# Performance work log

Hardware: AMD Instinct MI355X
Metric: run time of the kernel (lower is better)

## Reference

```python
import jax, jax.numpy as jnp
import numpy as np

DIM = 512  # DIM_IMAGE_EMBEDDING
HEAD = 64
B, T = 16, 2048


def setup_inputs() -> dict:
    key = jax.random.key(0)
    ks = jax.random.split(key, 8)
    s = 1.0 / np.sqrt(DIM)
    return {
        'x': jax.random.normal(ks[0], (B, T, DIM), jnp.float32),
        'Wq': jax.random.normal(ks[1], (HEAD, DIM), jnp.float32) * s,
        'Wk': jax.random.normal(ks[2], (HEAD, DIM), jnp.float32) * s,
        'Wv': jax.random.normal(ks[3], (HEAD, DIM), jnp.float32) * s,
        'fx_real': jax.random.normal(ks[4], (T, HEAD // 4), jnp.float32),
        'fx_imag': jax.random.normal(ks[5], (T, HEAD // 4), jnp.float32),
        'fy_real': jax.random.normal(ks[6], (T, HEAD // 4), jnp.float32),
        'fy_imag': jax.random.normal(ks[7], (T, HEAD // 4), jnp.float32),
    }


def _rotate_half(t, fr, fi):
    # t: [B, T, H/2] viewed as H/4 complex pairs; fr, fi: [T, H/4]
    b, s, d = t.shape
    tc = t.reshape(b, s, d // 2, 2)
    a, bb = tc[..., 0], tc[..., 1]
    ro = a * fr - bb * fi  # real part of complex product
    io = a * fi + bb * fr  # imag part
    return jnp.stack([ro, io], axis=-1).reshape(b, s, d)


def apply_rotary_2d(t, fx_real, fx_imag, fy_real, fy_imag):
    h = t.shape[-1] // 2
    vx = _rotate_half(t[..., :h], fx_real, fx_imag)
    vy = _rotate_half(t[..., h:], fy_real, fy_imag)
    return jnp.concatenate([vx, vy], axis=-1)


def reference(x, Wq, Wk, Wv, fx_real, fx_imag, fy_real, fy_imag):
    C = x.shape[-1]
    q = jnp.einsum('btc,hc->bth', x, Wq)
    k = jnp.einsum('btc,hc->bth', x, Wk)
    v = jnp.einsum('btc,hc->bth', x, Wv)
    q = apply_rotary_2d(q, fx_real, fx_imag, fy_real, fy_imag)
    k = apply_rotary_2d(k, fx_real, fx_imag, fy_real, fy_imag)
    # NOTE: original scales by input dim C (=512), not head_size
    wei = jnp.einsum('bqh,bkh->bqk', q, k) / jnp.sqrt(jnp.float32(C))
    softwei = jax.nn.softmax(wei, axis=-1)
    out = jnp.einsum('bqk,bkh->bqh', softwei, v)
    return out
```

## Files before the change

kernel.cpp:

```cpp
#include <hip/hip_runtime.h>
#include <hip/hip_bf16.h>

#define BB 16
#define TT 2048
#define DIMC 512
#define HEADH 64

typedef __attribute__((ext_vector_type(8))) short short8v;
typedef __attribute__((ext_vector_type(4))) float f32x4;

static __device__ __forceinline__ unsigned short f2bf(float f) {
    __hip_bfloat16 h = __float2bfloat16(f);
    unsigned short u;
    __builtin_memcpy(&u, &h, 2);
    return u;
}
static __device__ __forceinline__ unsigned int packbf(float lo, float hi) {
    float2 f2; f2.x = lo; f2.y = hi;
    __hip_bfloat162 h2 = __float22bfloat162_rn(f2);
    unsigned int u;
    __builtin_memcpy(&u, &h2, 4);
    return u;
}
#define EXP2R __builtin_amdgcn_exp2f
static __device__ __forceinline__ void async_copy16(void* lds, const void* g) {
    __builtin_amdgcn_global_load_lds(
        (const __attribute__((address_space(1))) unsigned char*)g,
        (__attribute__((address_space(3))) unsigned char*)lds, 16, 0, 0);
}

union bfrag {
    unsigned int u[4];
    short8v v;
};

__global__ __launch_bounds__(256) void wcvt_kernel(
    const float* __restrict__ Wq, const float* __restrict__ Wk,
    const float* __restrict__ Wv, unsigned short* __restrict__ wb)
{
    const int idx = blockIdx.x * 256 + threadIdx.x;
    const int e   = idx << 3;
    const int row = e >> 9, col = e & 511;
    const float* src = (row < 64) ? Wq : (row < 128) ? Wk : Wv;
    const float* p = src + (size_t)(row & 63) * DIMC + col;
    float4 a = *(const float4*)p;
    float4 b = *(const float4*)(p + 4);
    uint4 o;
    o.x = packbf(a.x, a.y); o.y = packbf(a.z, a.w);
    o.z = packbf(b.x, b.y); o.w = packbf(b.z, b.w);
    *(uint4*)(wb + e) = o;
}

__global__ __launch_bounds__(256, 2) void qkv_mfma_kernel(
    const float* __restrict__ x,
    const unsigned short* __restrict__ wb,
    const float* __restrict__ fxr, const float* __restrict__ fxi,
    const float* __restrict__ fyr, const float* __restrict__ fyi,
    unsigned short* __restrict__ qo, unsigned short* __restrict__ ko,
    unsigned short* __restrict__ vt)
{
    __shared__ unsigned char xlds[16384];

    const int tid = threadIdx.x;
    const int w   = tid >> 6;
    const int l   = tid & 63;
    const int q   = l & 15;
    const int g   = l >> 4;
    const int t0  = blockIdx.x << 6;

    f32x4 acc[3][4];
    #pragma unroll
    for (int j = 0; j < 3; ++j)
        #pragma unroll
        for (int tt = 0; tt < 4; ++tt) acc[j][tt] = (f32x4){0.f, 0.f, 0.f, 0.f};

    const unsigned short* wp0 = wb + ((size_t)((3 * w + 0) * 16 + q)) * DIMC + 8 * g;
    const unsigned short* wp1 = wb + ((size_t)((3 * w + 1) * 16 + q)) * DIMC + 8 * g;
    const unsigned short* wp2 = wb + ((size_t)((3 * w + 2) * 16 + q)) * DIMC + 8 * g;

    const int rl = l >> 3;
    const int cb = (l & 7) ^ rl;
    const float* xsrc0 = x + (size_t)(t0 + 16 * w + 0 + rl) * DIMC + 4 * cb;
    const float* xsrc1 = x + (size_t)(t0 + 16 * w + 8 + rl) * DIMC + 4 * cb;
    unsigned char* xdst0 = xlds + (16 * w + 0) * 128;
    unsigned char* xdst1 = xlds + (16 * w + 8) * 128;

#define STAGE_X(bufsel, k0) do {                                              \
        async_copy16(xdst0 + (bufsel) * 8192, xsrc0 + (k0));                  \
        async_copy16(xdst1 + (bufsel) * 8192, xsrc1 + (k0));                  \
    } while (0)

    STAGE_X(0, 0);
    __syncthreads();

    int cur = 0;
    for (int it = 0; it < 16; ++it) {
        const int k0 = it << 5;
        if (it < 15) STAGE_X(cur ^ 1, k0 + 32);

        short8v wf0 = *(const short8v*)(wp0 + k0);
        short8v wf1 = *(const short8v*)(wp1 + k0);
        short8v wf2 = *(const short8v*)(wp2 + k0);

        const unsigned char* xb = xlds + cur * 8192;
        #pragma unroll
        for (int tt = 0; tt < 4; ++tt) {
            const int rr = tt * 16 + q;
            const int s0 = (2 * g)     ^ (q & 7);
            const int s1 = (2 * g + 1) ^ (q & 7);
            float4 f0 = *(const float4*)(xb + rr * 128 + s0 * 16);
            float4 f1 = *(const float4*)(xb + rr * 128 + s1 * 16);
            bfrag xv;
            xv.u[0] = packbf(f0.x, f0.y); xv.u[1] = packbf(f0.z, f0.w);
            xv.u[2] = packbf(f1.x, f1.y); xv.u[3] = packbf(f1.z, f1.w);
            acc[0][tt] = __builtin_amdgcn_mfma_f32_16x16x32_bf16(wf0, xv.v, acc[0][tt], 0, 0, 0);
            acc[1][tt] = __builtin_amdgcn_mfma_f32_16x16x32_bf16(wf1, xv.v, acc[1][tt], 0, 0, 0);
            acc[2][tt] = __builtin_amdgcn_mfma_f32_16x16x32_bf16(wf2, xv.v, acc[2][tt], 0, 0, 0);
        }

        __syncthreads();
        cur ^= 1;
    }

    const float qscale = 1.4426950408889634f / 22.627416997969522f;
    #pragma unroll
    for (int j = 0; j < 3; ++j) {
        const int gt   = 3 * w + j;
        const int mat  = gt >> 2;
        const int hbase = (gt & 3) * 16 + 4 * g;
        #pragma unroll
        for (int tt = 0; tt < 4; ++tt) {
            const int trow = t0 + tt * 16 + q;
            const int tl   = trow & (TT - 1);
            if (mat == 2) {
                const int b = trow >> 11;
                #pragma unroll
                for (int r = 0; r < 4; ++r)
                    vt[((size_t)(b * HEADH) + hbase + r) * TT + tl] = f2bf(acc[j][tt][r]);
            } else {
                const float sc = (mat == 0) ? qscale : 1.f;
                unsigned short* dst = ((mat == 0) ? qo : ko) + (size_t)trow * HEADH;
                const int half = hbase >> 5;
                const float* frt = half ? fyr : fxr;
                const float* fit = half ? fyi : fxi;
                const int pi0 = (hbase & 31) >> 1;
                float fr0 = frt[tl * 16 + pi0],     fi0 = fit[tl * 16 + pi0];
                float fr1 = frt[tl * 16 + pi0 + 1], fi1 = fit[tl * 16 + pi0 + 1];
                float e0 = acc[j][tt][0] * fr0 - acc[j][tt][1] * fi0;
                float e1 = acc[j][tt][0] * fi0 + acc[j][tt][1] * fr0;
                float e2 = acc[j][tt][2] * fr1 - acc[j][tt][3] * fi1;
                float e3 = acc[j][tt][2] * fi1 + acc[j][tt][3] * fr1;
                uint2 ow;
                ow.x = packbf(e0 * sc, e1 * sc);
                ow.y = packbf(e2 * sc, e3 * sc);
                *(uint2*)(dst + hbase) = ow;
            }
        }
    }
#undef STAGE_X
}

__global__ __launch_bounds__(256, 2) void attn_mfma_kernel(
    const unsigned short* __restrict__ qws,
    const unsigned short* __restrict__ kws,
    const unsigned short* __restrict__ vtw,
    float* __restrict__ out)
{
    __shared__ unsigned char smem[40960];

    const int tid = threadIdx.x;
    const int w   = tid >> 6;
    const int l   = tid & 63;
    const int q   = l & 15;
    const int g   = l >> 4;
    const int b   = blockIdx.x >> 5;
    const int q0  = (blockIdx.x & 31) << 6;
    const int qw  = q0 + 16 * w;
    const int rx  = q & 7;
    const int swz = (q & 7) << 2;

    const int rl = l >> 3;
    const int sl = (l & 7) ^ rl;

    unsigned int* pldsw = (unsigned int*)(smem + 32768 + (w << 11));

    const unsigned short* kbase = kws + (size_t)b * TT * HEADH;
    const unsigned short* vbase = vtw + (size_t)b * HEADH * TT;

    const unsigned short* ksrc0 = kbase + (size_t)(16 * w + rl) * HEADH + 8 * sl;
    const unsigned short* ksrc1 = kbase + (size_t)(16 * w + 8 + rl) * HEADH + 8 * sl;
    const unsigned short* vsrc0 = vbase + (size_t)(16 * w + rl) * TT + 8 * sl;
    const unsigned short* vsrc1 = vbase + (size_t)(16 * w + 8 + rl) * TT + 8 * sl;

#define STAGE_TILE(bufsel, kv)  do {                                          \
        unsigned char* kd = smem + (bufsel) * 8192 + (w << 11);               \
        unsigned char* vd = smem + 16384 + (bufsel) * 8192 + (w << 11);       \
        async_copy16(kd,        ksrc0 + (size_t)(kv) * HEADH);                \
        async_copy16(kd + 1024, ksrc1 + (size_t)(kv) * HEADH);                \
        async_copy16(vd,        vsrc0 + (kv));                                \
        async_copy16(vd + 1024, vsrc1 + (kv));                                \
    } while (0)

    short8v qf0, qf1;
    {
        const unsigned short* qp = qws + ((size_t)(b * TT + qw + q)) * HEADH + 8 * g;
        qf0 = *(const short8v*)(qp);
        qf1 = *(const short8v*)(qp + 32);
    }

    f32x4 oacc[4];
    #pragma unroll
    for (int mt = 0; mt < 4; ++mt) oacc[mt] = (f32x4){0.f, 0.f, 0.f, 0.f};
    float m = -1e30f, lsum = 0.f;

    STAGE_TILE(0, 0);
    __syncthreads();

    int cur = 0;
    for (int it = 0; it < 32; ++it) {
        if (it < 31) STAGE_TILE(cur ^ 1, (it + 1) << 6);

        const unsigned char* kb = smem + cur * 8192;
        const unsigned char* vb = smem + 16384 + cur * 8192;

        f32x4 sacc[4];
        #pragma unroll
        for (int n = 0; n < 4; ++n) {
            const int r = 16 * n + q;
            const short8v k0 = *(const short8v*)(kb + r * 128 + ((g ^ rx) << 4));
            const short8v k1 = *(const short8v*)(kb + r * 128 + (((4 + g) ^ rx) << 4));
            f32x4 z = (f32x4){0.f, 0.f, 0.f, 0.f};
            z = __builtin_amdgcn_mfma_f32_16x16x32_bf16(k0, qf0, z, 0, 0, 0);
            z = __builtin_amdgcn_mfma_f32_16x16x32_bf16(k1, qf1, z, 0, 0, 0);
            sacc[n] = z;
        }

        float cmax = sacc[0][0];
        #pragma unroll
        for (int n = 0; n < 4; ++n)
            #pragma unroll
            for (int r = 0; r < 4; ++r) cmax = fmaxf(cmax, sacc[n][r]);
        cmax = fmaxf(cmax, __shfl_xor(cmax, 16));
        cmax = fmaxf(cmax, __shfl_xor(cmax, 32));
        const float mnew = fmaxf(m, cmax);

        float p[4][4];
        float psum = 0.f;
        #pragma unroll
        for (int n = 0; n < 4; ++n)
            #pragma unroll
            for (int r = 0; r < 4; ++r) {
                p[n][r] = EXP2R(sacc[n][r] - mnew);
                psum += p[n][r];
            }
        psum += __shfl_xor(psum, 16);
        psum += __shfl_xor(psum, 32);

        const float sc = EXP2R(m - mnew);
        if (__any(cmax > m)) {
            #pragma unroll
            for (int mt = 0; mt < 4; ++mt)
                #pragma unroll
                for (int r = 0; r < 4; ++r) oacc[mt][r] *= sc;
        }
        lsum = lsum * sc + psum;
        m = mnew;

        #pragma unroll
        for (int n = 0; n < 4; ++n) {
            uint2 wv;
            wv.x = packbf(p[n][0], p[n][1]);
            wv.y = packbf(p[n][2], p[n][3]);
            *(uint2*)&pldsw[q * 32 + ((8 * n + 2 * g) ^ swz)] = wv;
        }

        #pragma unroll
        for (int s = 0; s < 2; ++s) {
            const short8v pb = *(const short8v*)&pldsw[q * 32 + ((16 * s + 4 * g) ^ swz)];
            #pragma unroll
            for (int mt = 0; mt < 4; ++mt) {
                const int d = 16 * mt + q;
                const short8v vfr = *(const short8v*)(vb + d * 128 + ((((s << 2) + g) ^ rx) << 4));
                oacc[mt] = __builtin_amdgcn_mfma_f32_16x16x32_bf16(vfr, pb, oacc[mt], 0, 0, 0);
            }
        }

        __syncthreads();
        cur ^= 1;
    }

    const float inv = 1.f / lsum;
    float* op = out + ((size_t)(b * TT + qw + q)) * HEADH;
    #pragma unroll
    for (int mt = 0; mt < 4; ++mt) {
        float4 v4 = make_float4(oacc[mt][0] * inv, oacc[mt][1] * inv,
                                oacc[mt][2] * inv, oacc[mt][3] * inv);
        *(float4*)(op + 16 * mt + 4 * g) = v4;
    }
#undef STAGE_TILE
}

extern "C" void kernel_launch(void* const* d_in, const int* in_sizes, int n_in,
                              void* d_out, int out_size, void* d_ws, size_t ws_size,
                              hipStream_t stream)
{
    const float* x   = (const float*)d_in[0];
    const float* Wq  = (const float*)d_in[1];
    const float* Wk  = (const float*)d_in[2];
    const float* Wv  = (const float*)d_in[3];
    const float* fxr = (const float*)d_in[4];
    const float* fxi = (const float*)d_in[5];
    const float* fyr = (const float*)d_in[6];
    const float* fyi = (const float*)d_in[7];
    float* out = (float*)d_out;

    unsigned short* qo = (unsigned short*)d_ws;
    unsigned short* ko = qo + (size_t)BB * TT * HEADH;
    unsigned short* vt = ko + (size_t)BB * TT * HEADH;
    unsigned short* wb = vt + (size_t)BB * TT * HEADH;

    wcvt_kernel<<<48, 256, 0, stream>>>(Wq, Wk, Wv, wb);
    qkv_mfma_kernel<<<(BB * TT) / 64, 256, 0, stream>>>(x, wb, fxr, fxi, fyr, fyi,
                                                        qo, ko, vt);
    attn_mfma_kernel<<<BB * 32, 256, 0, stream>>>(qo, ko, vt, out);
}
```

Measured before the change: 71.74 us.

## Load V fragments directly from global memory and raise attention occupancy

The attention kernel no longer stages V tiles through LDS. Each lane loads its V fragments straight from global memory into registers at the start of every iteration. This shrinks shared memory from 40KB to 24KB, and launch bounds go from 2 to 4 blocks per CU. The softmax row-sum reduction is also moved after the PV MFMAs so it can overlap them. The risk is global-load latency on the critical path before the PV MFMAs, and more register pressure under the tighter launch bound.

```diff
diff --git a/kernel.cpp b/kernel.cpp
--- a/kernel.cpp
+++ b/kernel.cpp
@@ -160,13 +160,13 @@
 #undef STAGE_X
 }
 
-__global__ __launch_bounds__(256, 2) void attn_mfma_kernel(
+__global__ __launch_bounds__(256, 4) void attn_mfma_kernel(
     const unsigned short* __restrict__ qws,
     const unsigned short* __restrict__ kws,
     const unsigned short* __restrict__ vtw,
     float* __restrict__ out)
 {
-    __shared__ unsigned char smem[40960];
+    __shared__ unsigned char smem[24576];
 
     const int tid = threadIdx.x;
     const int w   = tid >> 6;
@@ -182,23 +182,18 @@
     const int rl = l >> 3;
     const int sl = (l & 7) ^ rl;
 
-    unsigned int* pldsw = (unsigned int*)(smem + 32768 + (w << 11));
+    unsigned int* pldsw = (unsigned int*)(smem + 16384 + (w << 11));
 
     const unsigned short* kbase = kws + (size_t)b * TT * HEADH;
     const unsigned short* vbase = vtw + (size_t)b * HEADH * TT;
 
     const unsigned short* ksrc0 = kbase + (size_t)(16 * w + rl) * HEADH + 8 * sl;
     const unsigned short* ksrc1 = kbase + (size_t)(16 * w + 8 + rl) * HEADH + 8 * sl;
-    const unsigned short* vsrc0 = vbase + (size_t)(16 * w + rl) * TT + 8 * sl;
-    const unsigned short* vsrc1 = vbase + (size_t)(16 * w + 8 + rl) * TT + 8 * sl;
-
-#define STAGE_TILE(bufsel, kv)  do {                                          \
+
+#define STAGE_K(bufsel, kv)  do {                                             \
         unsigned char* kd = smem + (bufsel) * 8192 + (w << 11);               \
-        unsigned char* vd = smem + 16384 + (bufsel) * 8192 + (w << 11);       \
         async_copy16(kd,        ksrc0 + (size_t)(kv) * HEADH);                \
         async_copy16(kd + 1024, ksrc1 + (size_t)(kv) * HEADH);                \
-        async_copy16(vd,        vsrc0 + (kv));                                \
-        async_copy16(vd + 1024, vsrc1 + (kv));                                \
     } while (0)
 
     short8v qf0, qf1;
@@ -213,15 +208,23 @@
     for (int mt = 0; mt < 4; ++mt) oacc[mt] = (f32x4){0.f, 0.f, 0.f, 0.f};
     float m = -1e30f, lsum = 0.f;
 
-    STAGE_TILE(0, 0);
+    STAGE_K(0, 0);
     __syncthreads();
 
     int cur = 0;
     for (int it = 0; it < 32; ++it) {
-        if (it < 31) STAGE_TILE(cur ^ 1, (it + 1) << 6);
+        const int kv0 = it << 6;
+        if (it < 31) STAGE_K(cur ^ 1, kv0 + 64);
+
+        short8v vf[2][4];
+        #pragma unroll
+        for (int s = 0; s < 2; ++s)
+            #pragma unroll
+            for (int mt = 0; mt < 4; ++mt)
+                vf[s][mt] = *(const short8v*)(vbase +
+                    (size_t)(16 * mt + q) * TT + kv0 + 32 * s + 8 * g);
 
         const unsigned char* kb = smem + cur * 8192;
-        const unsigned char* vb = smem + 16384 + cur * 8192;
 
         f32x4 sacc[4];
         #pragma unroll
@@ -245,45 +248,43 @@
         const float mnew = fmaxf(m, cmax);
 
         float p[4][4];
-        float psum = 0.f;
-        #pragma unroll
-        for (int n = 0; n < 4; ++n)
-            #pragma unroll
-            for (int r = 0; r < 4; ++r) {
+        #pragma unroll
+        for (int n = 0; n < 4; ++n) {
+            #pragma unroll
+            for (int r = 0; r < 4; ++r)
                 p[n][r] = EXP2R(sacc[n][r] - mnew);
-                psum += p[n][r];
-            }
-        psum += __shfl_xor(psum, 16);
-        psum += __shfl_xor(psum, 32);
-
-        const float sc = EXP2R(m - mnew);
-        if (__any(cmax > m)) {
-            #pragma unroll
-            for (int mt = 0; mt < 4; ++mt)
-                #pragma unroll
-                for (int r = 0; r < 4; ++r) oacc[mt][r] *= sc;
-        }
-        lsum = lsum * sc + psum;
-        m = mnew;
-
-        #pragma unroll
-        for (int n = 0; n < 4; ++n) {
             uint2 wv;
             wv.x = packbf(p[n][0], p[n][1]);
             wv.y = packbf(p[n][2], p[n][3]);
             *(uint2*)&pldsw[q * 32 + ((8 * n + 2 * g) ^ swz)] = wv;
         }
 
+        const float sc = EXP2R(m - mnew);
+        if (__any(cmax > m)) {
+            #pragma unroll
+            for (int mt = 0; mt < 4; ++mt)
+                #pragma unroll
+                for (int r = 0; r < 4; ++r) oacc[mt][r] *= sc;
+        }
+
         #pragma unroll
         for (int s = 0; s < 2; ++s) {
             const short8v pb = *(const short8v*)&pldsw[q * 32 + ((16 * s + 4 * g) ^ swz)];
             #pragma unroll
-            for (int mt = 0; mt < 4; ++mt) {
-                const int d = 16 * mt + q;
-                const short8v vfr = *(const short8v*)(vb + d * 128 + ((((s << 2) + g) ^ rx) << 4));
-                oacc[mt] = __builtin_amdgcn_mfma_f32_16x16x32_bf16(vfr, pb, oacc[mt], 0, 0, 0);
-            }
-        }
+            for (int mt = 0; mt < 4; ++mt)
+                oacc[mt] = __builtin_amdgcn_mfma_f32_16x16x32_bf16(vf[s][mt], pb,
+                                                                   oacc[mt], 0, 0, 0);
+        }
+
+        float psum = 0.f;
+        #pragma unroll
+        for (int n = 0; n < 4; ++n)
+            #pragma unroll
+            for (int r = 0; r < 4; ++r) psum += p[n][r];
+        psum += __shfl_xor(psum, 16);
+        psum += __shfl_xor(psum, 32);
+        lsum = lsum * sc + psum;
+        m = mnew;
 
         __syncthreads();
         cur ^= 1;
@@ -297,7 +298,7 @@
                                 oacc[mt][2] * inv, oacc[mt][3] * inv);
         *(float4*)(op + 16 * mt + 4 * g) = v4;
     }
-#undef STAGE_TILE
+#undef STAGE_K
 }
 
 extern "C" void kernel_launch(void* const* d_in, const int* in_sizes, int n_in,
```

Result: slower. 97.07 us (+35.3%).

## Split attention KV range across two wave groups and halve QKV tile rows

Applied to the files above, without the earlier changes.

The attention kernel now runs 512 threads per block: two groups of four waves each handle half of the key/value sequence for the same 64 queries. Their partial softmax states (max, sum, output) are merged through shared memory at the end. The QKV projection kernel is retiled to 32 tokens per block, doubling the grid and raising the occupancy hint. Together these aim to expose more parallelism and latency hiding on 512 attention blocks, at the cost of doubled LDS use in attention and an extra merge phase. The softmax row-sum is also moved after the PV MFMAs so it can overlap with them.

```diff
diff --git a/kernel.cpp b/kernel.cpp
--- a/kernel.cpp
+++ b/kernel.cpp
@@ -51,7 +51,7 @@
     *(uint4*)(wb + e) = o;
 }
 
-__global__ __launch_bounds__(256, 2) void qkv_mfma_kernel(
+__global__ __launch_bounds__(256, 4) void qkv_mfma_kernel(
     const float* __restrict__ x,
     const unsigned short* __restrict__ wb,
     const float* __restrict__ fxr, const float* __restrict__ fxi,
@@ -59,20 +59,20 @@
     unsigned short* __restrict__ qo, unsigned short* __restrict__ ko,
     unsigned short* __restrict__ vt)
 {
-    __shared__ unsigned char xlds[16384];
+    __shared__ unsigned char xlds[8192];
 
     const int tid = threadIdx.x;
     const int w   = tid >> 6;
     const int l   = tid & 63;
     const int q   = l & 15;
     const int g   = l >> 4;
-    const int t0  = blockIdx.x << 6;
-
-    f32x4 acc[3][4];
+    const int t0  = blockIdx.x << 5;
+
+    f32x4 acc[3][2];
     #pragma unroll
     for (int j = 0; j < 3; ++j)
         #pragma unroll
-        for (int tt = 0; tt < 4; ++tt) acc[j][tt] = (f32x4){0.f, 0.f, 0.f, 0.f};
+        for (int tt = 0; tt < 2; ++tt) acc[j][tt] = (f32x4){0.f, 0.f, 0.f, 0.f};
 
     const unsigned short* wp0 = wb + ((size_t)((3 * w + 0) * 16 + q)) * DIMC + 8 * g;
     const unsigned short* wp1 = wb + ((size_t)((3 * w + 1) * 16 + q)) * DIMC + 8 * g;
@@ -80,15 +80,11 @@
 
     const int rl = l >> 3;
     const int cb = (l & 7) ^ rl;
-    const float* xsrc0 = x + (size_t)(t0 + 16 * w + 0 + rl) * DIMC + 4 * cb;
-    const float* xsrc1 = x + (size_t)(t0 + 16 * w + 8 + rl) * DIMC + 4 * cb;
-    unsigned char* xdst0 = xlds + (16 * w + 0) * 128;
-    unsigned char* xdst1 = xlds + (16 * w + 8) * 128;
-
-#define STAGE_X(bufsel, k0) do {                                              \
-        async_copy16(xdst0 + (bufsel) * 8192, xsrc0 + (k0));                  \
-        async_copy16(xdst1 + (bufsel) * 8192, xsrc1 + (k0));                  \
-    } while (0)
+    const float* xsrc = x + (size_t)(t0 + 8 * w + rl) * DIMC + 4 * cb;
+    unsigned char* xdst = xlds + (w << 10);
+
+#define STAGE_X(bufsel, k0) \
+        async_copy16(xdst + (bufsel) * 4096, xsrc + (k0))
 
     STAGE_X(0, 0);
     __syncthreads();
@@ -102,9 +98,9 @@
         short8v wf1 = *(const short8v*)(wp1 + k0);
         short8v wf2 = *(const short8v*)(wp2 + k0);
 
-        const unsigned char* xb = xlds + cur * 8192;
-        #pragma unroll
-        for (int tt = 0; tt < 4; ++tt) {
+        const unsigned char* xb = xlds + cur * 4096;
+        #pragma unroll
+        for (int tt = 0; tt < 2; ++tt) {
             const int rr = tt * 16 + q;
             const int s0 = (2 * g)     ^ (q & 7);
             const int s1 = (2 * g + 1) ^ (q & 7);
@@ -129,7 +125,7 @@
         const int mat  = gt >> 2;
         const int hbase = (gt & 3) * 16 + 4 * g;
         #pragma unroll
-        for (int tt = 0; tt < 4; ++tt) {
+        for (int tt = 0; tt < 2; ++tt) {
             const int trow = t0 + tt * 16 + q;
             const int tl   = trow & (TT - 1);
             if (mat == 2) {
@@ -160,43 +156,45 @@
 #undef STAGE_X
 }
 
-__global__ __launch_bounds__(256, 2) void attn_mfma_kernel(
+__global__ __launch_bounds__(512, 4) void attn_mfma_kernel(
     const unsigned short* __restrict__ qws,
     const unsigned short* __restrict__ kws,
     const unsigned short* __restrict__ vtw,
     float* __restrict__ out)
 {
-    __shared__ unsigned char smem[40960];
+    __shared__ unsigned char smem[81920];
 
     const int tid = threadIdx.x;
     const int w   = tid >> 6;
+    const int wq  = w & 3;
+    const int h   = w >> 2;
     const int l   = tid & 63;
     const int q   = l & 15;
     const int g   = l >> 4;
     const int b   = blockIdx.x >> 5;
     const int q0  = (blockIdx.x & 31) << 6;
-    const int qw  = q0 + 16 * w;
+    const int qw  = q0 + 16 * wq;
     const int rx  = q & 7;
     const int swz = (q & 7) << 2;
 
     const int rl = l >> 3;
     const int sl = (l & 7) ^ rl;
 
-    unsigned int* pldsw = (unsigned int*)(smem + 32768 + (w << 11));
+    unsigned int* pldsw = (unsigned int*)(smem + 65536 + (w << 11));
 
     const unsigned short* kbase = kws + (size_t)b * TT * HEADH;
     const unsigned short* vbase = vtw + (size_t)b * HEADH * TT;
 
-    const unsigned short* ksrc0 = kbase + (size_t)(16 * w + rl) * HEADH + 8 * sl;
-    const unsigned short* ksrc1 = kbase + (size_t)(16 * w + 8 + rl) * HEADH + 8 * sl;
-    const unsigned short* vsrc0 = vbase + (size_t)(16 * w + rl) * TT + 8 * sl;
-    const unsigned short* vsrc1 = vbase + (size_t)(16 * w + 8 + rl) * TT + 8 * sl;
+    const unsigned short* ksrc0 = kbase + (size_t)(h * 1024 + 16 * wq + rl) * HEADH + 8 * sl;
+    const unsigned short* ksrc1 = ksrc0 + (size_t)8 * HEADH;
+    const unsigned short* vsrc0 = vbase + (size_t)(16 * wq + rl) * TT + h * 1024 + 8 * sl;
+    const unsigned short* vsrc1 = vsrc0 + (size_t)8 * TT;
 
 #define STAGE_TILE(bufsel, kv)  do {                                          \
-        unsigned char* kd = smem + (bufsel) * 8192 + (w << 11);               \
-        unsigned char* vd = smem + 16384 + (bufsel) * 8192 + (w << 11);       \
+        unsigned char* kd = smem + (h << 14) + (bufsel) * 8192 + (wq << 11);  \
         async_copy16(kd,        ksrc0 + (size_t)(kv) * HEADH);                \
         async_copy16(kd + 1024, ksrc1 + (size_t)(kv) * HEADH);                \
+        unsigned char* vd = smem + 32768 + (h << 14) + (bufsel) * 8192 + (wq << 11); \
         async_copy16(vd,        vsrc0 + (kv));                                \
         async_copy16(vd + 1024, vsrc1 + (kv));                                \
     } while (0)
@@ -217,11 +215,12 @@
     __syncthreads();
 
     int cur = 0;
-    for (int it = 0; it < 32; ++it) {
-        if (it < 31) STAGE_TILE(cur ^ 1, (it + 1) << 6);
-
-        const unsigned char* kb = smem + cur * 8192;
-        const unsigned char* vb = smem + 16384 + cur * 8192;
+    for (int it = 0; it < 16; ++it) {
+        const int kv0 = it << 6;
+        if (it < 15) STAGE_TILE(cur ^ 1, kv0 + 64);
+
+        const unsigned char* kb = smem + (h << 14) + cur * 8192;
+        const unsigned char* vb = smem + 32768 + (h << 14) + cur * 8192;
 
         f32x4 sacc[4];
         #pragma unroll
@@ -245,33 +244,23 @@
         const float mnew = fmaxf(m, cmax);
 
         float p[4][4];
-        float psum = 0.f;
-        #pragma unroll
-        for (int n = 0; n < 4; ++n)
-            #pragma unroll
-            for (int r = 0; r < 4; ++r) {
+        #pragma unroll
+        for (int n = 0; n < 4; ++n) {
+            #pragma unroll
+            for (int r = 0; r < 4; ++r)
                 p[n][r] = EXP2R(sacc[n][r] - mnew);
-                psum += p[n][r];
-            }
-        psum += __shfl_xor(psum, 16);
-        psum += __shfl_xor(psum, 32);
-
-        const float sc = EXP2R(m - mnew);
-        if (__any(cmax > m)) {
-            #pragma unroll
-            for (int mt = 0; mt < 4; ++mt)
-                #pragma unroll
-                for (int r = 0; r < 4; ++r) oacc[mt][r] *= sc;
-        }
-        lsum = lsum * sc + psum;
-        m = mnew;
-
-        #pragma unroll
-        for (int n = 0; n < 4; ++n) {
             uint2 wv;
             wv.x = packbf(p[n][0], p[n][1]);
             wv.y = packbf(p[n][2], p[n][3]);
             *(uint2*)&pldsw[q * 32 + ((8 * n + 2 * g) ^ swz)] = wv;
+        }
+
+        const float sc = EXP2R(m - mnew);
+        if (__any(cmax > m)) {
+            #pragma unroll
+            for (int mt = 0; mt < 4; ++mt)
+                #pragma unroll
+                for (int r = 0; r < 4; ++r) oacc[mt][r] *= sc;
         }
 
         #pragma unroll
@@ -285,18 +274,55 @@
             }
         }
 
+        float psum = 0.f;
+        #pragma unroll
+        for (int n = 0; n < 4; ++n)
+            #pragma unroll
+            for (int r = 0; r < 4; ++r) psum += p[n][r];
+        psum += __shfl_xor(psum, 16);
+        psum += __shfl_xor(psum, 32);
+        lsum = lsum * sc + psum;
+        m = mnew;
+
         __syncthreads();
         cur ^= 1;
     }
 
-    const float inv = 1.f / lsum;
-    float* op = out + ((size_t)(b * TT + qw + q)) * HEADH;
-    #pragma unroll
-    for (int mt = 0; mt < 4; ++mt) {
-        float4 v4 = make_float4(oacc[mt][0] * inv, oacc[mt][1] * inv,
-                                oacc[mt][2] * inv, oacc[mt][3] * inv);
-        *(float4*)(op + 16 * mt + 4 * g) = v4;
-    }
+    __syncthreads();
+    float* o_f  = (float*)smem;
+    float* ml_f = (float*)(smem + 32768);
+    {
+        const int prow = h * 64 + 16 * wq + q;
+        #pragma unroll
+        for (int mt = 0; mt < 4; ++mt)
+            *(f32x4*)&o_f[prow * 64 + 16 * mt + 4 * g] = oacc[mt];
+        if (g == 0) {
+            ml_f[h * 128 + 16 * wq + q]      = m;
+            ml_f[h * 128 + 64 + 16 * wq + q] = lsum;
+        }
+    }
+    __syncthreads();
+
+    const int cq = tid >> 3;
+    const int ch = (tid & 7) << 3;
+    const float m0 = ml_f[cq],       l0 = ml_f[64 + cq];
+    const float m1 = ml_f[128 + cq], l1 = ml_f[192 + cq];
+    const float M  = fmaxf(m0, m1);
+    const float a0 = EXP2R(m0 - M), a1 = EXP2R(m1 - M);
+    const float inv = 1.f / (a0 * l0 + a1 * l1);
+    const float* o0 = &o_f[cq * 64 + ch];
+    const float* o1 = &o_f[(64 + cq) * 64 + ch];
+    float4 A0 = *(const float4*)(o0), B0 = *(const float4*)(o0 + 4);
+    float4 A1 = *(const float4*)(o1), B1 = *(const float4*)(o1 + 4);
+    float* op = out + ((size_t)(b * TT + q0 + cq)) * HEADH + ch;
+    *(float4*)(op)     = make_float4((a0 * A0.x + a1 * A1.x) * inv,
+                                     (a0 * A0.y + a1 * A1.y) * inv,
+                                     (a0 * A0.z + a1 * A1.z) * inv,
+                                     (a0 * A0.w + a1 * A1.w) * inv);
+    *(float4*)(op + 4) = make_float4((a0 * B0.x + a1 * B1.x) * inv,
+                                     (a0 * B0.y + a1 * B1.y) * inv,
+                                     (a0 * B0.z + a1 * B1.z) * inv,
+                                     (a0 * B0.w + a1 * B1.w) * inv);
 #undef STAGE_TILE
 }
 
@@ -320,7 +346,7 @@
     unsigned short* wb = vt + (size_t)BB * TT * HEADH;
 
     wcvt_kernel<<<48, 256, 0, stream>>>(Wq, Wk, Wv, wb);
-    qkv_mfma_kernel<<<(BB * TT) / 64, 256, 0, stream>>>(x, wb, fxr, fxi, fyr, fyi,
+    qkv_mfma_kernel<<<(BB * TT) / 32, 256, 0, stream>>>(x, wb, fxr, fxi, fyr, fyi,
                                                         qo, ko, vt);
-    attn_mfma_kernel<<<BB * 32, 256, 0, stream>>>(qo, ko, vt, out);
-}
+    attn_mfma_kernel<<<BB * 32, 512, 0, stream>>>(qo, ko, vt, out);
+}
```

Result: slower. 74.81 us (+4.3%).

## Split KV into four chunks per block with 32x32 MFMA and merge partial softmax

Applied to the files above, without the earlier changes.

The attention kernel now launches 512 threads per block: two query halves of 32 rows times four KV chunks of 512 keys each, an in-block split-K flash-decoding scheme. It uses 32x32x16 bf16 MFMAs instead of 16x16x32, and passes the P fragments through cross-lane shuffles instead of an LDS round trip. At the end, the per-chunk partial outputs, maxima and sums are merged through LDS. The aim is more waves per CU and fewer serial loop iterations per wave. In exchange it needs more LDS (about 66KB per block), adds an epilogue reduction, and relies on a `bfrag` type defined outside this hunk.

```diff
diff --git a/kernel.cpp b/kernel.cpp
--- a/kernel.cpp
+++ b/kernel.cpp
@@ -8,6 +8,7 @@
 
 typedef __attribute__((ext_vector_type(8))) short short8v;
 typedef __attribute__((ext_vector_type(4))) float f32x4;
+typedef __attribute__((ext_vector_type(16))) float f32x16;
 
 static __device__ __forceinline__ unsigned short f2bf(float f) {
     __hip_bfloat16 h = __float2bfloat16(f);
@@ -160,143 +161,192 @@
 #undef STAGE_X
 }
 
-__global__ __launch_bounds__(256, 2) void attn_mfma_kernel(
+__global__ __launch_bounds__(512, 4) void attn_mfma_kernel(
     const unsigned short* __restrict__ qws,
     const unsigned short* __restrict__ kws,
     const unsigned short* __restrict__ vtw,
     float* __restrict__ out)
 {
-    __shared__ unsigned char smem[40960];
+    __shared__ unsigned char smem[67584];
 
     const int tid = threadIdx.x;
     const int w   = tid >> 6;
+    const int wq  = w & 1;
+    const int h   = w >> 1;
     const int l   = tid & 63;
-    const int q   = l & 15;
-    const int g   = l >> 4;
+    const int q   = l & 31;
+    const int g5  = l >> 5;
     const int b   = blockIdx.x >> 5;
     const int q0  = (blockIdx.x & 31) << 6;
-    const int qw  = q0 + 16 * w;
-    const int rx  = q & 7;
-    const int swz = (q & 7) << 2;
-
-    const int rl = l >> 3;
-    const int sl = (l & 7) ^ rl;
-
-    unsigned int* pldsw = (unsigned int*)(smem + 32768 + (w << 11));
+    const int qb  = q0 + 32 * wq;
+
+    const int rl  = l >> 3;
+    const int skl = (l & 7) ^ rl;
+    const int rl4 = l >> 2;
+    const int svl = (l & 3) ^ (rl4 & 3);
 
     const unsigned short* kbase = kws + (size_t)b * TT * HEADH;
     const unsigned short* vbase = vtw + (size_t)b * HEADH * TT;
 
-    const unsigned short* ksrc0 = kbase + (size_t)(16 * w + rl) * HEADH + 8 * sl;
-    const unsigned short* ksrc1 = kbase + (size_t)(16 * w + 8 + rl) * HEADH + 8 * sl;
-    const unsigned short* vsrc0 = vbase + (size_t)(16 * w + rl) * TT + 8 * sl;
-    const unsigned short* vsrc1 = vbase + (size_t)(16 * w + 8 + rl) * TT + 8 * sl;
+    const unsigned short* ksrc = kbase + (size_t)(h * 512 + 16 * wq + rl) * HEADH + 8 * skl;
+    const unsigned short* vsrc = vbase + (size_t)(32 * wq + rl4) * TT + h * 512 + 8 * svl;
 
 #define STAGE_TILE(bufsel, kv)  do {                                          \
-        unsigned char* kd = smem + (bufsel) * 8192 + (w << 11);               \
-        unsigned char* vd = smem + 16384 + (bufsel) * 8192 + (w << 11);       \
-        async_copy16(kd,        ksrc0 + (size_t)(kv) * HEADH);                \
-        async_copy16(kd + 1024, ksrc1 + (size_t)(kv) * HEADH);                \
-        async_copy16(vd,        vsrc0 + (kv));                                \
-        async_copy16(vd + 1024, vsrc1 + (kv));                                \
+        unsigned char* kd = smem + h * 8192 + (bufsel) * 4096 + wq * 2048;    \
+        async_copy16(kd,        ksrc + (size_t)(kv) * HEADH);                 \
+        async_copy16(kd + 1024, ksrc + (size_t)((kv) + 8) * HEADH);           \
+        unsigned char* vd = smem + 32768 + h * 8192 + (bufsel) * 4096 + wq * 2048; \
+        async_copy16(vd,        vsrc + (kv));                                 \
+        async_copy16(vd + 1024, vsrc + (kv) + 16 * TT);                       \
     } while (0)
 
-    short8v qf0, qf1;
+    short8v qf[4];
     {
-        const unsigned short* qp = qws + ((size_t)(b * TT + qw + q)) * HEADH + 8 * g;
-        qf0 = *(const short8v*)(qp);
-        qf1 = *(const short8v*)(qp + 32);
-    }
-
-    f32x4 oacc[4];
-    #pragma unroll
-    for (int mt = 0; mt < 4; ++mt) oacc[mt] = (f32x4){0.f, 0.f, 0.f, 0.f};
+        const unsigned short* qp = qws + ((size_t)(b * TT + qb + q)) * HEADH + 8 * g5;
+        #pragma unroll
+        for (int kc = 0; kc < 4; ++kc) qf[kc] = *(const short8v*)(qp + 16 * kc);
+    }
+
+    f32x16 oacc[2];
+    #pragma unroll
+    for (int db = 0; db < 2; ++db)
+        #pragma unroll
+        for (int r = 0; r < 16; ++r) oacc[db][r] = 0.f;
     float m = -1e30f, lsum = 0.f;
 
     STAGE_TILE(0, 0);
     __syncthreads();
 
     int cur = 0;
-    for (int it = 0; it < 32; ++it) {
-        if (it < 31) STAGE_TILE(cur ^ 1, (it + 1) << 6);
-
-        const unsigned char* kb = smem + cur * 8192;
-        const unsigned char* vb = smem + 16384 + cur * 8192;
-
-        f32x4 sacc[4];
-        #pragma unroll
-        for (int n = 0; n < 4; ++n) {
-            const int r = 16 * n + q;
-            const short8v k0 = *(const short8v*)(kb + r * 128 + ((g ^ rx) << 4));
-            const short8v k1 = *(const short8v*)(kb + r * 128 + (((4 + g) ^ rx) << 4));
-            f32x4 z = (f32x4){0.f, 0.f, 0.f, 0.f};
-            z = __builtin_amdgcn_mfma_f32_16x16x32_bf16(k0, qf0, z, 0, 0, 0);
-            z = __builtin_amdgcn_mfma_f32_16x16x32_bf16(k1, qf1, z, 0, 0, 0);
-            sacc[n] = z;
-        }
-
-        float cmax = sacc[0][0];
-        #pragma unroll
-        for (int n = 0; n < 4; ++n)
-            #pragma unroll
-            for (int r = 0; r < 4; ++r) cmax = fmaxf(cmax, sacc[n][r]);
-        cmax = fmaxf(cmax, __shfl_xor(cmax, 16));
+    for (int it = 0; it < 16; ++it) {
+        const int kv0 = it << 5;
+        if (it < 15) STAGE_TILE(cur ^ 1, kv0 + 32);
+
+        const unsigned char* kb = smem + h * 8192 + cur * 4096;
+        const unsigned char* vb = smem + 32768 + h * 8192 + cur * 4096;
+
+        f32x16 sacc;
+        #pragma unroll
+        for (int r = 0; r < 16; ++r) sacc[r] = 0.f;
+        #pragma unroll
+        for (int kc = 0; kc < 4; ++kc) {
+            const short8v kA = *(const short8v*)(kb + q * 128 +
+                                   (((2 * kc + g5) ^ (q & 7)) << 4));
+            sacc = __builtin_amdgcn_mfma_f32_32x32x16_bf16(kA, qf[kc], sacc, 0, 0, 0);
+        }
+
+        float t0a = fmaxf(fmaxf(sacc[0], sacc[1]),   fmaxf(sacc[2], sacc[3]));
+        float t1a = fmaxf(fmaxf(sacc[4], sacc[5]),   fmaxf(sacc[6], sacc[7]));
+        float t2a = fmaxf(fmaxf(sacc[8], sacc[9]),   fmaxf(sacc[10], sacc[11]));
+        float t3a = fmaxf(fmaxf(sacc[12], sacc[13]), fmaxf(sacc[14], sacc[15]));
+        float cmax = fmaxf(fmaxf(t0a, t1a), fmaxf(t2a, t3a));
         cmax = fmaxf(cmax, __shfl_xor(cmax, 32));
         const float mnew = fmaxf(m, cmax);
 
-        float p[4][4];
-        float psum = 0.f;
-        #pragma unroll
-        for (int n = 0; n < 4; ++n)
-            #pragma unroll
-            for (int r = 0; r < 4; ++r) {
-                p[n][r] = EXP2R(sacc[n][r] - mnew);
-                psum += p[n][r];
-            }
-        psum += __shfl_xor(psum, 16);
-        psum += __shfl_xor(psum, 32);
+        float p[16];
+        #pragma unroll
+        for (int r = 0; r < 16; ++r) p[r] = EXP2R(sacc[r] - mnew);
+
+        unsigned int W0 = packbf(p[0],  p[1]),  W1 = packbf(p[2],  p[3]);
+        unsigned int W2 = packbf(p[4],  p[5]),  W3 = packbf(p[6],  p[7]);
+        unsigned int W4 = packbf(p[8],  p[9]),  W5 = packbf(p[10], p[11]);
+        unsigned int W6 = packbf(p[12], p[13]), W7 = packbf(p[14], p[15]);
+
+        const unsigned int X0 = __shfl_xor(W0, 32);
+        const unsigned int X1 = __shfl_xor(W1, 32);
+        const unsigned int X2 = __shfl_xor(W2, 32);
+        const unsigned int X3 = __shfl_xor(W3, 32);
+        const unsigned int X4 = __shfl_xor(W4, 32);
+        const unsigned int X5 = __shfl_xor(W5, 32);
+        const unsigned int X6 = __shfl_xor(W6, 32);
+        const unsigned int X7 = __shfl_xor(W7, 32);
+        bfrag pb0, pb1;
+        pb0.u[0] = g5 ? X2 : W0;
+        pb0.u[1] = g5 ? X3 : W1;
+        pb0.u[2] = g5 ? W2 : X0;
+        pb0.u[3] = g5 ? W3 : X1;
+        pb1.u[0] = g5 ? X6 : W4;
+        pb1.u[1] = g5 ? X7 : W5;
+        pb1.u[2] = g5 ? W6 : X4;
+        pb1.u[3] = g5 ? W7 : X5;
 
         const float sc = EXP2R(m - mnew);
         if (__any(cmax > m)) {
             #pragma unroll
-            for (int mt = 0; mt < 4; ++mt)
+            for (int db = 0; db < 2; ++db)
                 #pragma unroll
-                for (int r = 0; r < 4; ++r) oacc[mt][r] *= sc;
-        }
+                for (int r = 0; r < 16; ++r) oacc[db][r] *= sc;
+        }
+
+        #pragma unroll
+        for (int db = 0; db < 2; ++db) {
+            const int d = 32 * db + q;
+            const short8v vA0 = *(const short8v*)(vb + d * 64 + (((g5) ^ (d & 3)) << 4));
+            oacc[db] = __builtin_amdgcn_mfma_f32_32x32x16_bf16(vA0, pb0.v, oacc[db], 0, 0, 0);
+            const short8v vA1 = *(const short8v*)(vb + d * 64 + (((2 + g5) ^ (d & 3)) << 4));
+            oacc[db] = __builtin_amdgcn_mfma_f32_32x32x16_bf16(vA1, pb1.v, oacc[db], 0, 0, 0);
+        }
+
+        float psum = 0.f;
+        #pragma unroll
+        for (int r = 0; r < 16; ++r) psum += p[r];
+        psum += __shfl_xor(psum, 32);
         lsum = lsum * sc + psum;
         m = mnew;
 
-        #pragma unroll
-        for (int n = 0; n < 4; ++n) {
-            uint2 wv;
-            wv.x = packbf(p[n][0], p[n][1]);
-            wv.y = packbf(p[n][2], p[n][3]);
-            *(uint2*)&pldsw[q * 32 + ((8 * n + 2 * g) ^ swz)] = wv;
-        }
-
-        #pragma unroll
-        for (int s = 0; s < 2; ++s) {
-            const short8v pb = *(const short8v*)&pldsw[q * 32 + ((16 * s + 4 * g) ^ swz)];
-            #pragma unroll
-            for (int mt = 0; mt < 4; ++mt) {
-                const int d = 16 * mt + q;
-                const short8v vfr = *(const short8v*)(vb + d * 128 + ((((s << 2) + g) ^ rx) << 4));
-                oacc[mt] = __builtin_amdgcn_mfma_f32_16x16x32_bf16(vfr, pb, oacc[mt], 0, 0, 0);
-            }
-        }
-
         __syncthreads();
         cur ^= 1;
     }
 
-    const float inv = 1.f / lsum;
-    float* op = out + ((size_t)(b * TT + qw + q)) * HEADH;
-    #pragma unroll
-    for (int mt = 0; mt < 4; ++mt) {
-        float4 v4 = make_float4(oacc[mt][0] * inv, oacc[mt][1] * inv,
-                                oacc[mt][2] * inv, oacc[mt][3] * inv);
-        *(float4*)(op + 16 * mt + 4 * g) = v4;
-    }
+    __syncthreads();
+    float* o_f  = (float*)smem;
+    float* ml_f = (float*)(smem + 65536);
+    {
+        const int qrow = 32 * wq + q;
+        #pragma unroll
+        for (int db = 0; db < 2; ++db)
+            #pragma unroll
+            for (int rq = 0; rq < 4; ++rq) {
+                float4 v = make_float4(oacc[db][4 * rq], oacc[db][4 * rq + 1],
+                                       oacc[db][4 * rq + 2], oacc[db][4 * rq + 3]);
+                *(float4*)&o_f[(h * 64 + qrow) * 64 + 32 * db + 8 * rq + 4 * g5] = v;
+            }
+        if (l < 32) {
+            ml_f[h * 128 + 32 * wq + l]      = m;
+            ml_f[h * 128 + 64 + 32 * wq + l] = lsum;
+        }
+    }
+    __syncthreads();
+
+    const int cq = tid >> 3;
+    const int ch = (tid & 7) << 3;
+    float mh[4], lh[4];
+    #pragma unroll
+    for (int hh = 0; hh < 4; ++hh) {
+        mh[hh] = ml_f[hh * 128 + cq];
+        lh[hh] = ml_f[hh * 128 + 64 + cq];
+    }
+    const float M = fmaxf(fmaxf(mh[0], mh[1]), fmaxf(mh[2], mh[3]));
+    float den = 0.f;
+    float num[8];
+    #pragma unroll
+    for (int j = 0; j < 8; ++j) num[j] = 0.f;
+    #pragma unroll
+    for (int hh = 0; hh < 4; ++hh) {
+        const float al = EXP2R(mh[hh] - M);
+        den += al * lh[hh];
+        const float* ov = &o_f[(hh * 64 + cq) * 64 + ch];
+        float4 v0 = *(const float4*)(ov);
+        float4 v1 = *(const float4*)(ov + 4);
+        num[0] += al * v0.x; num[1] += al * v0.y;
+        num[2] += al * v0.z; num[3] += al * v0.w;
+        num[4] += al * v1.x; num[5] += al * v1.y;
+        num[6] += al * v1.z; num[7] += al * v1.w;
+    }
+    const float inv = 1.f / den;
+    float* op = out + ((size_t)(b * TT + q0 + cq)) * HEADH + ch;
+    *(float4*)(op)     = make_float4(num[0] * inv, num[1] * inv, num[2] * inv, num[3] * inv);
+    *(float4*)(op + 4) = make_float4(num[4] * inv, num[5] * inv, num[6] * inv, num[7] * inv);
 #undef STAGE_TILE
 }
 
@@ -322,5 +372,5 @@
     wcvt_kernel<<<48, 256, 0, stream>>>(Wq, Wk, Wv, wb);
     qkv_mfma_kernel<<<(BB * TT) / 64, 256, 0, stream>>>(x, wb, fxr, fxi, fyr, fyi,
                                                         qo, ko, vt);
-    attn_mfma_kernel<<<BB * 32, 256, 0, stream>>>(qo, ko, vt, out);
-}
+    attn_mfma_kernel<<<BB * 32, 512, 0, stream>>>(qo, ko, vt, out);
+}
```

Result: slower. 73.92 us (+3.0%).
